# Kernel optimization log

Hardware: AMD Instinct MI355X
Metric: run time of the kernel (lower is better)

Reference implementation:

```python
import jax, jax.numpy as jnp
import numpy as np

BN_EPS = 1e-5
KNN_K = 9
HEAD = 4


def _bn(x, gamma, beta, axis=1):
    # eval-mode BatchNorm with running_mean=0, running_var=1
    shape = [1] * x.ndim
    shape[axis] = -1
    scale = (gamma / jnp.sqrt(1.0 + BN_EPS)).reshape(shape)
    return x * scale + beta.reshape(shape)


def _conv1d(x, W, b):
    # 1x1 Conv1d == channel matmul; x: [B,C,N], W: [O,C], b: [O]
    return jnp.einsum('oc,bcn->bon', W, x) + b[None, :, None]


def _knn_idx(x, k):
    # x: [B,C,N] -> idx [B,N,k] of k nearest (incl. self)
    xx = jnp.sum(x * x, axis=1)                      # [B,N]
    inner = jnp.einsum('bcn,bcm->bnm', x, x)         # [B,N,N]
    neg_d = 2.0 * inner - xx[:, :, None] - xx[:, None, :]
    return jax.lax.top_k(neg_d, k)[1]


def _graph_feature(x, k):
    # x: [B,C,N] -> [B,2C,N,k]  (cat of center feature and center - neighbor)
    B, C, N = x.shape
    idx = _knn_idx(x, k)                             # [B,N,k]
    xt = jnp.transpose(x, (0, 2, 1))                 # [B,N,C]
    nbr = jax.vmap(lambda xb, ib: xb[ib])(xt, idx)   # [B,N,k,C]
    ctr = jnp.broadcast_to(xt[:, :, None, :], (B, N, k, C))
    feat = jnp.concatenate([ctr, ctr - nbr], axis=3)  # [B,N,k,2C]
    return jnp.transpose(feat, (0, 3, 1, 2))


def _dgcnn_max(x, w1, b1, g1, be1, w2, b2, g2, be2, k):
    # x: [B,C,N] -> [B,C,N]; two 1x1 convs + BN + ReLU then max over k
    ef = _graph_feature(x, k)                        # [B,2C,N,k]
    h = jnp.einsum('oc,bcnk->bonk', w1, ef) + b1[None, :, None, None]
    h = jax.nn.relu(_bn(h, g1, be1, axis=1))
    h = jnp.einsum('oc,bcnk->bonk', w2, h) + b2[None, :, None, None]
    h = jax.nn.relu(_bn(h, g2, be2, axis=1))
    return jnp.max(h, axis=-1)                       # [B,C,N]


def _attention(m1, m2, wq, bq, wk, bk, wv, bv, wmh, bmh, wc1, bc1, cg, cbe, wc2, bc2):
    B, C, N = m1.shape
    hd = C // HEAD
    q = _conv1d(m1, wq, bq).reshape(B, HEAD, hd, N)
    kk = _conv1d(m2, wk, bk).reshape(B, HEAD, hd, -1)
    v = _conv1d(m2, wv, bv).reshape(B, HEAD, hd, -1)
    score = jax.nn.softmax(jnp.einsum('bhdn,bhdm->bhnm', q, kk) / (float(hd) ** 0.5), axis=-1)
    add = jnp.einsum('bhnm,bhdm->bhdn', score, v).reshape(B, C, N)
    add = _conv1d(add, wmh, bmh)
    cat = jnp.concatenate([m1, add], axis=1)         # [B,2C,N]
    h = jax.nn.relu(_bn(_conv1d(cat, wc1, bc1), cg, cbe, axis=1))
    return m1 + _conv1d(h, wc2, bc2)


def setup_inputs() -> dict:
    key = jax.random.key(0)
    B, C, N = 4, 128, 2000
    ks = jax.random.split(key, 24)

    def w(k, shape, s=0.05):
        return jax.random.normal(k, shape, dtype=jnp.float32) * s

    inp = {
        'x': jax.random.normal(ks[0], (B, C, N, 1), dtype=jnp.float32),
        'y': jax.random.normal(ks[1], (B, C, N), dtype=jnp.float32),
        # DGCNN_MAX_Block conv params (two 1x1 Conv2d + BN)
        'dg_w1': w(ks[2], (C, 2 * C)), 'dg_b1': w(ks[3], (C,)),
        'dg_g1': jnp.ones((C,), jnp.float32), 'dg_be1': jnp.zeros((C,), jnp.float32),
        'dg_w2': w(ks[4], (C, C)), 'dg_b2': w(ks[5], (C,)),
        'dg_g2': jnp.ones((C,), jnp.float32), 'dg_be2': jnp.zeros((C,), jnp.float32),
        # AttentionPropagation params
        'wq': w(ks[6], (C, C)), 'bq': w(ks[7], (C,)),
        'wk': w(ks[8], (C, C)), 'bk': w(ks[9], (C,)),
        'wv': w(ks[10], (C, C)), 'bv': w(ks[11], (C,)),
        'wmh': w(ks[12], (C, C)), 'bmh': w(ks[13], (C,)),
        'wc1': w(ks[14], (2 * C, 2 * C)), 'bc1': w(ks[15], (2 * C,)),
        'cg': jnp.ones((2 * C,), jnp.float32), 'cbe': jnp.zeros((2 * C,), jnp.float32),
        'wc2': w(ks[16], (C, 2 * C)), 'bc2': w(ks[17], (C,)),
    }
    return inp


def reference(x, y, dg_w1, dg_b1, dg_g1, dg_be1, dg_w2, dg_b2, dg_g2, dg_be2,
              wq, bq, wk, bk, wv, bv, wmh, bmh, wc1, bc1, cg, cbe, wc2, bc2):
    feats = x[:, :, :, 0]                            # [B,C,N]
    agg = _dgcnn_max(feats, dg_w1, dg_b1, dg_g1, dg_be1,
                     dg_w2, dg_b2, dg_g2, dg_be2, KNN_K)
    out = _attention(agg, y, wq, bq, wk, bk, wv, bv, wmh, bmh,
                     wc1, bc1, cg, cbe, wc2, bc2)
    return out[:, :, :, None]                        # [B,C,N,1]
```

## Files before the change

### kernel.cpp

```cpp
#include <hip/hip_runtime.h>

#define BATCH 4
#define CH    128
#define NPTS  2000
#define KNN   9
#define NHEAD 4
#define HD    32

typedef unsigned short u16;
typedef __attribute__((ext_vector_type(4))) float f32x4;
typedef __attribute__((ext_vector_type(8))) short bf16x8;

#define OFF_XT    0
#define OFF_YT    1024000
#define OFF_PT    2048000
#define OFF_QT    3072000
#define OFF_AGG   4096000
#define OFF_MH    5120000
#define OFF_MISC  6144000
#define OFF_W1SUM (OFF_MISC)
#define OFF_W1B   (OFF_MISC+16384)
#define OFF_W2T   (OFF_MISC+32768)
#define OFF_WC1T  (OFF_MISC+114688)
#define OFF_B1F   (OFF_MISC+212992)
#define OFF_B2F   (OFF_MISC+213120)
#define OFF_BC1F  (OFF_MISC+213248)
#define OFF_XX    (OFF_MISC+213504)
#define OFF_IDX   (OFF_MISC+221504)

__device__ __forceinline__ void bsplit(float v, u16& hi, u16& lo)
{
    unsigned u = __float_as_uint(v);
    unsigned h16 = (u + 0x7fffu + ((u >> 16) & 1u)) >> 16;
    float hf = __uint_as_float(h16 << 16);
    float lf = v - hf;
    unsigned ul = __float_as_uint(lf);
    hi = (u16)h16;
    lo = (u16)((ul + 0x7fffu + ((ul >> 16) & 1u)) >> 16);
}

__device__ __forceinline__ f32x4 mfma16(bf16x8 a, bf16x8 b, f32x4 c)
{
    return __builtin_amdgcn_mfma_f32_16x16x32_bf16(a, b, c, 0, 0, 0);
}

__global__ __launch_bounds__(256) void prep_kernel(
    const float* __restrict__ w1, const float* __restrict__ b1,
    const float* __restrict__ g1, const float* __restrict__ be1,
    const float* __restrict__ w2, const float* __restrict__ b2,
    const float* __restrict__ g2, const float* __restrict__ be2,
    const float* __restrict__ wc1, const float* __restrict__ bc1,
    const float* __restrict__ cg, const float* __restrict__ cbe,
    float* __restrict__ ws)
{
    int id = blockIdx.x * 256 + threadIdx.x;
    const float rs = rsqrtf(1.f + 1e-5f);
    if (id < 16384) {
        int o = id >> 7, c = id & 127;
        float s1 = g1[o] * rs;
        ws[OFF_W1SUM + id] = (w1[o*256 + c] + w1[o*256 + 128 + c]) * s1;
        ws[OFF_W1B   + id] = w1[o*256 + 128 + c] * s1;
        ws[OFF_W2T   + id] = w2[id] * (g2[o] * rs);
    }
    {
        int o = id >> 8;
        ws[OFF_WC1T + id] = wc1[id] * (cg[o] * rs);
    }
    if (id < 128) {
        float s1 = g1[id] * rs, s2 = g2[id] * rs;
        ws[OFF_B1F + id] = b1[id]*s1 + be1[id];
        ws[OFF_B2F + id] = b2[id]*s2 + be2[id];
    }
    if (id < 256) {
        ws[OFF_BC1F + id] = bc1[id]*(cg[id]*rs) + cbe[id];
    }
}

__global__ __launch_bounds__(128) void transpose_split_kernel(
    const float* __restrict__ src, float* __restrict__ dst, float* __restrict__ xx,
    u16* __restrict__ H, u16* __restrict__ L)
{
    int blk = blockIdx.x; int b = blk / NPTS, n = blk % NPTS;
    int c = threadIdx.x;
    float v = src[((size_t)b*CH + c)*NPTS + n];
    size_t di = ((size_t)b*NPTS + n)*CH + c;
    dst[di] = v;
    u16 hi, lo;
    bsplit(v, hi, lo);
    H[di] = hi; L[di] = lo;
    __shared__ float red[128];
    red[c] = v*v;
    __syncthreads();
    for (int s = 64; s > 0; s >>= 1) { if (c < s) red[c] += red[c+s]; __syncthreads(); }
    if (c == 0) xx[b*NPTS + n] = red[0];
}

__global__ __launch_bounds__(128) void transpose_kernel(
    const float* __restrict__ src, float* __restrict__ dst)
{
    int blk = blockIdx.x; int b = blk / NPTS, n = blk % NPTS;
    int c = threadIdx.x;
    dst[((size_t)b*NPTS + n)*CH + c] = src[((size_t)b*CH + c)*NPTS + n];
}

__global__ __launch_bounds__(512) void knn8_kernel(
    const u16* __restrict__ XH, const u16* __restrict__ XL,
    const float* __restrict__ xx, int* __restrict__ idxOut)
{
    __shared__ float woutv[8][16][9];
    __shared__ int   wouti[8][16][9];
    int b = blockIdx.y;
    int q0 = blockIdx.x * 16;
    int tid = threadIdx.x;
    int wave = tid >> 6, lane = tid & 63;
    int lg = lane >> 4, lr = lane & 15;
    const float* xxb = xx + (size_t)b*NPTS;

    size_t qb = ((size_t)b*NPTS + q0 + lr)*128 + lg*8;
    bf16x8 qh[4], ql[4];
#pragma unroll
    for (int ch = 0; ch < 4; ch++) {
        qh[ch] = *(const bf16x8*)&XH[qb + ch*32];
        ql[ch] = *(const bf16x8*)&XL[qb + ch*32];
    }

    float vals[4][9]; int ids[4][9];
    float vmin[4]; int amin[4];
#pragma unroll
    for (int j = 0; j < 4; j++) {
#pragma unroll
        for (int k = 0; k < 9; k++) { vals[j][k] = -3.4e38f; ids[j][k] = -1; }
        vmin[j] = -3.4e38f; amin[j] = 0;
    }

    for (int t = wave; t < 125; t += 8) {
        size_t kb = ((size_t)b*NPTS + t*16 + lr)*128 + lg*8;
        bf16x8 fh[4], fl[4];
#pragma unroll
        for (int ch = 0; ch < 4; ch++) {
            fh[ch] = *(const bf16x8*)&XH[kb + ch*32];
            fl[ch] = *(const bf16x8*)&XL[kb + ch*32];
        }
        float xv = xxb[t*16 + lr];
        f32x4 acc = {0.f,0.f,0.f,0.f};
#pragma unroll
        for (int ch = 0; ch < 4; ch++) {
            acc = mfma16(qh[ch], fh[ch], acc);
            acc = mfma16(qh[ch], fl[ch], acc);
            acc = mfma16(ql[ch], fh[ch], acc);
            acc = mfma16(ql[ch], fl[ch], acc);
        }
        int cand = t*16 + lr;
#pragma unroll
        for (int j = 0; j < 4; j++) {
            float s = 2.f*acc[j] - xv;
            if (s > vmin[j]) {
#pragma unroll
                for (int k = 0; k < 9; k++) {
                    bool sel = (k == amin[j]);
                    vals[j][k] = sel ? s    : vals[j][k];
                    ids[j][k]  = sel ? cand : ids[j][k];
                }
                vmin[j] = vals[j][0]; amin[j] = 0;
#pragma unroll
                for (int k = 1; k < 9; k++) {
                    bool lt = vals[j][k] < vmin[j];
                    vmin[j] = lt ? vals[j][k] : vmin[j];
                    amin[j] = lt ? k : amin[j];
                }
            }
        }
    }

#pragma unroll
    for (int j = 0; j < 4; j++) {
        unsigned used = 0;
        for (int r = 0; r < 9; r++) {
            float bv = -3.4e38f; int bm = -1;
#pragma unroll
            for (int k = 0; k < 9; k++) {
                bool ok = !(used & (1u << k)) && (vals[j][k] > bv);
                bv = ok ? vals[j][k] : bv;
                bm = ok ? ids[j][k]  : bm;
            }
            float v = bv; int mi = bm;
#pragma unroll
            for (int off = 1; off < 16; off <<= 1) {
                float ov = __shfl_xor(v, off);
                int  omi = __shfl_xor(mi, off);
                if (ov > v || (ov == v && omi >= 0 && omi < mi)) { v = ov; mi = omi; }
            }
#pragma unroll
            for (int k = 0; k < 9; k++) {
                if (ids[j][k] == mi) used |= (1u << k);
            }
            if (lr == 0) { woutv[wave][lg*4+j][r] = v; wouti[wave][lg*4+j][r] = mi; }
        }
    }
    __syncthreads();

    if (tid < 16) {
        float v0 = woutv[0][tid][0], v1 = woutv[1][tid][0], v2 = woutv[2][tid][0], v3 = woutv[3][tid][0];
        float v4 = woutv[4][tid][0], v5 = woutv[5][tid][0], v6 = woutv[6][tid][0], v7 = woutv[7][tid][0];
        int   i0 = wouti[0][tid][0], i1 = wouti[1][tid][0], i2 = wouti[2][tid][0], i3 = wouti[3][tid][0];
        int   i4 = wouti[4][tid][0], i5 = wouti[5][tid][0], i6 = wouti[6][tid][0], i7 = wouti[7][tid][0];
        int   p0 = 1, p1 = 1, p2 = 1, p3 = 1, p4 = 1, p5 = 1, p6 = 1, p7 = 1;
        int* op = idxOut + ((size_t)b*NPTS + q0 + tid)*KNN;
        for (int r = 0; r < 9; r++) {
            int w = 0; float bv = v0; int bi = i0;
            if (v1 > bv || (v1 == bv && i1 < bi)) { w = 1; bv = v1; bi = i1; }
            if (v2 > bv || (v2 == bv && i2 < bi)) { w = 2; bv = v2; bi = i2; }
            if (v3 > bv || (v3 == bv && i3 < bi)) { w = 3; bv = v3; bi = i3; }
            if (v4 > bv || (v4 == bv && i4 < bi)) { w = 4; bv = v4; bi = i4; }
            if (v5 > bv || (v5 == bv && i5 < bi)) { w = 5; bv = v5; bi = i5; }
            if (v6 > bv || (v6 == bv && i6 < bi)) { w = 6; bv = v6; bi = i6; }
            if (v7 > bv || (v7 == bv && i7 < bi)) { w = 7; bv = v7; bi = i7; }
            op[r] = bi;
            if (w == 0)      { v0 = (p0 < 9) ? woutv[0][tid][p0] : -3.4e38f; i0 = (p0 < 9) ? wouti[0][tid][p0] : 0x7fffffff; p0++; }
            else if (w == 1) { v1 = (p1 < 9) ? woutv[1][tid][p1] : -3.4e38f; i1 = (p1 < 9) ? wouti[1][tid][p1] : 0x7fffffff; p1++; }
            else if (w == 2) { v2 = (p2 < 9) ? woutv[2][tid][p2] : -3.4e38f; i2 = (p2 < 9) ? wouti[2][tid][p2] : 0x7fffffff; p2++; }
            else if (w == 3) { v3 = (p3 < 9) ? woutv[3][tid][p3] : -3.4e38f; i3 = (p3 < 9) ? wouti[3][tid][p3] : 0x7fffffff; p3++; }
            else if (w == 4) { v4 = (p4 < 9) ? woutv[4][tid][p4] : -3.4e38f; i4 = (p4 < 9) ? wouti[4][tid][p4] : 0x7fffffff; p4++; }
            else if (w == 5) { v5 = (p5 < 9) ? woutv[5][tid][p5] : -3.4e38f; i5 = (p5 < 9) ? wouti[5][tid][p5] : 0x7fffffff; p5++; }
            else if (w == 6) { v6 = (p6 < 9) ? woutv[6][tid][p6] : -3.4e38f; i6 = (p6 < 9) ? wouti[6][tid][p6] : 0x7fffffff; p6++; }
            else             { v7 = (p7 < 9) ? woutv[7][tid][p7] : -3.4e38f; i7 = (p7 < 9) ? wouti[7][tid][p7] : 0x7fffffff; p7++; }
        }
    }
}

__global__ __launch_bounds__(128) void gemm_dual_kernel(
    const float* __restrict__ In, const float* __restrict__ Wa, const float* __restrict__ Wb,
    const float* __restrict__ ba, const float* __restrict__ bb,
    float* __restrict__ OutA, float* __restrict__ OutB)
{
    __shared__ float in_lds[8][128];
    int row0 = blockIdx.x * 8, tid = threadIdx.x;
    const float* src = In + (size_t)row0 * 128;
    for (int i = tid; i < 1024; i += 128) ((float*)in_lds)[i] = src[i];
    __syncthreads();
    float accA[8], accB[8];
    float bA = ba ? ba[tid] : 0.f, bB = bb ? bb[tid] : 0.f;
#pragma unroll
    for (int j = 0; j < 8; j++) { accA[j] = bA; accB[j] = bB; }
    const float4* wra = (const float4*)(Wa + (size_t)tid * 128);
    const float4* wrb = (const float4*)(Wb + (size_t)tid * 128);
#pragma unroll 4
    for (int c4 = 0; c4 < 32; c4++) {
        float4 wa = wra[c4], wb = wrb[c4];
#pragma unroll
        for (int j = 0; j < 8; j++) {
            float4 xi = ((const float4*)&in_lds[j][0])[c4];
            accA[j] += xi.x*wa.x + xi.y*wa.y + xi.z*wa.z + xi.w*wa.w;
            accB[j] += xi.x*wb.x + xi.y*wb.y + xi.z*wb.z + xi.w*wb.w;
        }
    }
#pragma unroll
    for (int j = 0; j < 8; j++) {
        OutA[(size_t)(row0 + j)*128 + tid] = accA[j];
        OutB[(size_t)(row0 + j)*128 + tid] = accB[j];
    }
}

__global__ __launch_bounds__(128) void gemm_kv_kernel(
    const float* __restrict__ In, const float* __restrict__ Wa, const float* __restrict__ Wb,
    const float* __restrict__ ba, const float* __restrict__ bb,
    u16* __restrict__ KHo, u16* __restrict__ KLo,
    u16* __restrict__ VTHo, u16* __restrict__ VTLo)
{
    __shared__ float in_lds[8][128];
    int row0 = blockIdx.x * 8, tid = threadIdx.x;
    const float* src = In + (size_t)row0 * 128;
    for (int i = tid; i < 1024; i += 128) ((float*)in_lds)[i] = src[i];
    __syncthreads();
    float accA[8], accB[8];
    float bA = ba[tid], bB = bb[tid];
#pragma unroll
    for (int j = 0; j < 8; j++) { accA[j] = bA; accB[j] = bB; }
    const float4* wra = (const float4*)(Wa + (size_t)tid * 128);
    const float4* wrb = (const float4*)(Wb + (size_t)tid * 128);
#pragma unroll 4
    for (int c4 = 0; c4 < 32; c4++) {
        float4 wa = wra[c4], wb = wrb[c4];
#pragma unroll
        for (int j = 0; j < 8; j++) {
            float4 xi = ((const float4*)&in_lds[j][0])[c4];
            accA[j] += xi.x*wa.x + xi.y*wa.y + xi.z*wa.z + xi.w*wa.w;
            accB[j] += xi.x*wb.x + xi.y*wb.y + xi.z*wb.z + xi.w*wb.w;
        }
    }
    int b = row0 / NPTS, n0 = row0 % NPTS;
#pragma unroll
    for (int j = 0; j < 8; j++) {
        u16 hh, ll;
        bsplit(accA[j], hh, ll);
        size_t ko = (size_t)(row0 + j)*128 + tid;
        KHo[ko] = hh; KLo[ko] = ll;
        bsplit(accB[j], hh, ll);
        size_t vo = ((size_t)b*128 + tid)*NPTS + n0 + j;
        VTHo[vo] = hh; VTLo[vo] = ll;
    }
}

__global__ __launch_bounds__(128) void gemm_q_kernel(
    const float* __restrict__ In, const float* __restrict__ Wt, const float* __restrict__ bias,
    u16* __restrict__ H, u16* __restrict__ L)
{
    __shared__ float in_lds[8][128];
    int row0 = blockIdx.x * 8, tid = threadIdx.x;
    const float* src = In + (size_t)row0 * 128;
    for (int i = tid; i < 1024; i += 128) ((float*)in_lds)[i] = src[i];
    __syncthreads();
    float acc[8];
    float b = bias[tid];
#pragma unroll
    for (int j = 0; j < 8; j++) acc[j] = b;
    const float4* wrow = (const float4*)(Wt + (size_t)tid * 128);
#pragma unroll 4
    for (int c4 = 0; c4 < 32; c4++) {
        float4 w = wrow[c4];
#pragma unroll
        for (int j = 0; j < 8; j++) {
            float4 xi = ((const float4*)&in_lds[j][0])[c4];
            acc[j] += xi.x*w.x + xi.y*w.y + xi.z*w.z + xi.w*w.w;
        }
    }
#pragma unroll
    for (int j = 0; j < 8; j++) {
        u16 hh, ll;
        bsplit(acc[j], hh, ll);
        size_t o = (size_t)(row0 + j)*128 + tid;
        H[o] = hh; L[o] = ll;
    }
}

template<int CIN, int COUT, bool RELU, bool TRANSOUT, bool HASRES, bool CONCAT>
__global__ __launch_bounds__(COUT) void gemmT_kernel(
    const float* __restrict__ In, const float* __restrict__ In2,
    const float* __restrict__ Wt, const float* __restrict__ bias,
    const float* __restrict__ Res, float* __restrict__ Out)
{
    __shared__ float in_lds[8][CIN];
    int row0 = blockIdx.x * 8, tid = threadIdx.x;
    if (!CONCAT) {
        const float* src = In + (size_t)row0 * CIN;
        for (int i = tid; i < 8*CIN; i += COUT) ((float*)in_lds)[i] = src[i];
    } else {
        for (int i = tid; i < 8*128; i += COUT) {
            int j = i >> 7, c = i & 127;
            in_lds[j][c]       = In [(size_t)(row0 + j)*128 + c];
            in_lds[j][128 + c] = In2[(size_t)(row0 + j)*128 + c];
        }
    }
    __syncthreads();
    float acc[8];
    float b = bias ? bias[tid] : 0.f;
#pragma unroll
    for (int j = 0; j < 8; j++) acc[j] = b;
    const float4* wrow = (const float4*)(Wt + (size_t)tid * CIN);
#pragma unroll 4
    for (int c4 = 0; c4 < CIN/4; c4++) {
        float4 w = wrow[c4];
#pragma unroll
        for (int j = 0; j < 8; j++) {
            float4 xi = ((const float4*)&in_lds[j][0])[c4];
            acc[j] += xi.x*w.x + xi.y*w.y + xi.z*w.z + xi.w*w.w;
        }
    }
#pragma unroll
    for (int j = 0; j < 8; j++) {
        float v = acc[j];
        if (RELU) v = fmaxf(v, 0.f);
        size_t row = row0 + j;
        if (HASRES) v += Res[row*COUT + tid];
        if (!TRANSOUT) {
            Out[row*COUT + tid] = v;
        } else {
            int b_ = (int)(row / NPTS), n_ = (int)(row % NPTS);
            Out[((size_t)b_*COUT + tid)*NPTS + n_] = v;
        }
    }
}

__global__ __launch_bounds__(128) void edgeconv_kernel(
    const float* __restrict__ Pt, const float* __restrict__ Qt,
    const int* __restrict__ idx, const float* __restrict__ W2t,
    const float* __restrict__ b2f, float* __restrict__ Agg)
{
    int blk = blockIdx.x; int b = blk / NPTS, n = blk % NPTS;
    int o = threadIdx.x;
    __shared__ float r[9][128];
    __shared__ int mk[9];
    if (o < 9) mk[o] = idx[((size_t)b*NPTS + n)*KNN + o];
    __syncthreads();
    float p = Pt[((size_t)b*NPTS + n)*128 + o];
#pragma unroll
    for (int k = 0; k < 9; k++) {
        float q = Qt[((size_t)b*NPTS + mk[k])*128 + o];
        r[k][o] = fmaxf(p - q, 0.f);
    }
    __syncthreads();
    float acc[9];
#pragma unroll
    for (int k = 0; k < 9; k++) acc[k] = 0.f;
    const float4* w2row = (const float4*)(W2t + (size_t)o * 128);
#pragma unroll 2
    for (int c4 = 0; c4 < 32; c4++) {
        float4 w = w2row[c4];
#pragma unroll
        for (int k = 0; k < 9; k++) {
            float4 rv = ((const float4*)&r[k][0])[c4];
            acc[k] += rv.x*w.x + rv.y*w.y + rv.z*w.z + rv.w*w.w;
        }
    }
    float bb = b2f[o];
    float vmax = -3.4e38f;
#pragma unroll
    for (int k = 0; k < 9; k++) vmax = fmaxf(vmax, fmaxf(acc[k] + bb, 0.f));
    Agg[((size_t)b*NPTS + n)*128 + o] = vmax;
}

#define PSTR 72
__global__ __launch_bounds__(256) void attn_mfma_kernel(
    const u16* __restrict__ QH, const u16* __restrict__ QL,
    const u16* __restrict__ KH, const u16* __restrict__ KL,
    const u16* __restrict__ VTH, const u16* __restrict__ VTL,
    float* __restrict__ Add)
{
    __shared__ alignas(16) u16 Ph[4][16][PSTR];
    __shared__ alignas(16) u16 Pl[4][16][PSTR];
    int b = blockIdx.z, h = blockIdx.y;
    int wave = threadIdx.x >> 6, lane = threadIdx.x & 63;
    int lg = lane >> 4, lr = lane & 15;
    int q0 = blockIdx.x * 64 + wave * 16;
    if (q0 >= NPTS) return;

    size_t qb = ((size_t)b*NPTS + q0 + lr)*128 + h*32 + lg*8;
    const bf16x8 qh = *(const bf16x8*)&QH[qb];
    const bf16x8 ql = *(const bf16x8*)&QL[qb];

    f32x4 o0 = {0.f,0.f,0.f,0.f}, o1 = {0.f,0.f,0.f,0.f};
    float mrun[4], lsum[4];
#pragma unroll
    for (int r = 0; r < 4; r++) { mrun[r] = -3.0e38f; lsum[r] = 0.f; }
    const float sc = 0.17677669529663687f;
    int shsrc = ((lr >> 2) << 4) | (lr & 3);

    for (int ks = 0; ks < NPTS; ks += 64) {
        f32x4 st[4];
        bool vk[4];
#pragma unroll
        for (int s = 0; s < 4; s++) {
            int key = ks + s*16 + lr;
            vk[s] = key < NPTS;
            int kc = key > NPTS-1 ? NPTS-1 : key;
            size_t kb = ((size_t)b*NPTS + kc)*128 + h*32 + lg*8;
            bf16x8 kh_ = *(const bf16x8*)&KH[kb];
            bf16x8 kl_ = *(const bf16x8*)&KL[kb];
            f32x4 ss = {0.f,0.f,0.f,0.f};
            ss = mfma16(qh, kh_, ss);
            ss = mfma16(qh, kl_, ss);
            ss = mfma16(ql, kh_, ss);
            st[s] = ss;
        }
        float mx[4];
#pragma unroll
        for (int r = 0; r < 4; r++) {
            float m_ = -3.0e38f;
#pragma unroll
            for (int s = 0; s < 4; s++) {
                float a = vk[s] ? st[s][r]*sc : -3.0e38f;
                st[s][r] = a;
                m_ = fmaxf(m_, a);
            }
            mx[r] = m_;
        }
#pragma unroll
        for (int off = 1; off < 16; off <<= 1) {
#pragma unroll
            for (int r = 0; r < 4; r++) mx[r] = fmaxf(mx[r], __shfl_xor(mx[r], off));
        }
        float sca[4], rsu[4];
        float e[4][4];
#pragma unroll
        for (int r = 0; r < 4; r++) {
            float mn = fmaxf(mrun[r], mx[r]);
            sca[r] = __expf(mrun[r] - mn);
            mrun[r] = mn;
            float su = 0.f;
#pragma unroll
            for (int s = 0; s < 4; s++) {
                float ev = __expf(st[s][r] - mn);
                e[s][r] = ev;
                su += ev;
            }
            rsu[r] = su;
        }
#pragma unroll
        for (int off = 1; off < 16; off <<= 1) {
#pragma unroll
            for (int r = 0; r < 4; r++) rsu[r] += __shfl_xor(rsu[r], off);
        }
#pragma unroll
        for (int r = 0; r < 4; r++) lsum[r] = lsum[r]*sca[r] + rsu[r];
#pragma unroll
        for (int r = 0; r < 4; r++) {
            int qr = lg*4 + r;
#pragma unroll
            for (int s = 0; s < 4; s++) {
                u16 hh, ll;
                bsplit(e[s][r], hh, ll);
                Ph[wave][qr][s*16 + lr] = hh;
                Pl[wave][qr][s*16 + lr] = ll;
            }
        }
        float scsel = (lr & 2) ? ((lr & 1) ? sca[3] : sca[2])
                               : ((lr & 1) ? sca[1] : sca[0]);
        float osc = __shfl(scsel, shsrc);
#pragma unroll
        for (int r = 0; r < 4; r++) { o0[r] *= osc; o1[r] *= osc; }
#pragma unroll
        for (int c = 0; c < 2; c++) {
            int cb = ks + c*32 + lg*8; if (cb > NPTS-8) cb = NPTS-8;
            bf16x8 pbh = *(const bf16x8*)&Ph[wave][lr][c*32 + lg*8];
            bf16x8 pbl = *(const bf16x8*)&Pl[wave][lr][c*32 + lg*8];
            size_t vb = ((size_t)b*128 + h*32 + lr)*NPTS + cb;
            bf16x8 v0h = *(const bf16x8*)&VTH[vb];
            bf16x8 v0l = *(const bf16x8*)&VTL[vb];
            bf16x8 v1h = *(const bf16x8*)&VTH[vb + 16*NPTS];
            bf16x8 v1l = *(const bf16x8*)&VTL[vb + 16*NPTS];
            o0 = mfma16(v0h, pbh, o0);
            o0 = mfma16(v0l, pbh, o0);
            o0 = mfma16(v0h, pbl, o0);
            o1 = mfma16(v1h, pbh, o1);
            o1 = mfma16(v1l, pbh, o1);
            o1 = mfma16(v1h, pbl, o1);
        }
    }
    float lsel = (lr & 2) ? ((lr & 1) ? lsum[3] : lsum[2])
                          : ((lr & 1) ? lsum[1] : lsum[0]);
    float rinv = 1.f / __shfl(lsel, shsrc);
    int q = q0 + lr;
    size_t ob = ((size_t)b*NPTS + q)*128 + h*32;
#pragma unroll
    for (int r = 0; r < 4; r++) {
        Add[ob + lg*4 + r]      = o0[r]*rinv;
        Add[ob + 16 + lg*4 + r] = o1[r]*rinv;
    }
}

extern "C" void kernel_launch(void* const* d_in, const int* in_sizes, int n_in,
                              void* d_out, int out_size, void* d_ws, size_t ws_size,
                              hipStream_t stream)
{
    const float* x    = (const float*)d_in[0];
    const float* y    = (const float*)d_in[1];
    const float* w1   = (const float*)d_in[2];
    const float* b1   = (const float*)d_in[3];
    const float* g1   = (const float*)d_in[4];
    const float* be1  = (const float*)d_in[5];
    const float* w2   = (const float*)d_in[6];
    const float* b2   = (const float*)d_in[7];
    const float* g2   = (const float*)d_in[8];
    const float* be2  = (const float*)d_in[9];
    const float* wq   = (const float*)d_in[10];
    const float* bq   = (const float*)d_in[11];
    const float* wk   = (const float*)d_in[12];
    const float* bk   = (const float*)d_in[13];
    const float* wv   = (const float*)d_in[14];
    const float* bv   = (const float*)d_in[15];
    const float* wmh  = (const float*)d_in[16];
    const float* bmh  = (const float*)d_in[17];
    const float* wc1  = (const float*)d_in[18];
    const float* bc1  = (const float*)d_in[19];
    const float* cg   = (const float*)d_in[20];
    const float* cbe  = (const float*)d_in[21];
    const float* wc2  = (const float*)d_in[22];
    const float* bc2  = (const float*)d_in[23];
    float* ws = (float*)d_ws;
    float* out = (float*)d_out;

    float* XT  = ws + OFF_XT;
    float* YT  = ws + OFF_YT;
    float* PT  = ws + OFF_PT;
    float* QT  = ws + OFF_QT;
    float* AGG = ws + OFF_AGG;
    float* MH  = ws + OFF_MH;
    float* XX  = ws + OFF_XX;
    int*   IDX = (int*)(ws + OFF_IDX);
    float* ADD = YT;
    float* TT  = PT;
    const int SPE = BATCH*NPTS*CH;
    u16* XHs = (u16*)MH;  u16* XLs = XHs + SPE;
    u16* QHs = (u16*)MH;  u16* QLs = QHs + SPE;
    u16* KHs = (u16*)QT;  u16* KLs = KHs + SPE;
    u16* VTH = (u16*)PT;  u16* VTL = VTH + SPE;

    prep_kernel<<<256, 256, 0, stream>>>(w1, b1, g1, be1, w2, b2, g2, be2,
                                         wc1, bc1, cg, cbe, ws);
    transpose_split_kernel<<<BATCH*NPTS, 128, 0, stream>>>(x, XT, XX, XHs, XLs);
    transpose_kernel<<<BATCH*NPTS, 128, 0, stream>>>(y, YT);
    knn8_kernel<<<dim3(NPTS/16, BATCH), 512, 0, stream>>>(XHs, XLs, XX, IDX);
    gemm_dual_kernel<<<BATCH*NPTS/8, 128, 0, stream>>>(XT, ws + OFF_W1SUM, ws + OFF_W1B,
                                                       ws + OFF_B1F, nullptr, PT, QT);
    edgeconv_kernel<<<BATCH*NPTS, 128, 0, stream>>>(PT, QT, IDX, ws + OFF_W2T,
                                                    ws + OFF_B2F, AGG);
    gemm_q_kernel<<<BATCH*NPTS/8, 128, 0, stream>>>(AGG, wq, bq, QHs, QLs);
    gemm_kv_kernel<<<BATCH*NPTS/8, 128, 0, stream>>>(YT, wk, wv, bk, bv,
                                                     KHs, KLs, VTH, VTL);
    attn_mfma_kernel<<<dim3(32, NHEAD, BATCH), 256, 0, stream>>>(
        QHs, QLs, KHs, KLs, VTH, VTL, ADD);
    gemmT_kernel<128,128,false,false,false,false><<<BATCH*NPTS/8, 128, 0, stream>>>(
        ADD, nullptr, wmh, bmh, nullptr, MH);
    gemmT_kernel<256,256,true,false,false,true><<<BATCH*NPTS/8, 256, 0, stream>>>(
        AGG, MH, ws + OFF_WC1T, ws + OFF_BC1F, nullptr, TT);
    gemmT_kernel<256,128,false,true,true,false><<<BATCH*NPTS/8, 128, 0, stream>>>(
        TT, nullptr, wc2, bc2, AGG, out);
}
```

Baseline: 569.0 us.

## Split attention keys in two halves with merge kernel; halve GEMM row tiles

The attention kernel now splits the 2000 keys into two halves processed by separate blocks, writing unnormalized partial outputs plus running max/sum, and a new merge kernel combines them flash-decoding style. The attention inner loop is narrowed from 64 to 32 keys per step. All the row-tiled fp32 GEMM kernels process 4 rows per block instead of 8, doubling block counts. The intent is more parallelism and occupancy for the attention grid (128→256 blocks per batch-head set). The cost is an extra kernel, extra global traffic for partials, and less weight reuse per block in the GEMMs.

```diff
diff --git a/kernel.cpp b/kernel.cpp
--- a/kernel.cpp
+++ b/kernel.cpp
@@ -6,6 +6,7 @@
 #define KNN   9
 #define NHEAD 4
 #define HD    32
+#define NHALF 1000
 
 typedef unsigned short u16;
 typedef __attribute__((ext_vector_type(4))) float f32x4;
@@ -21,6 +22,7 @@
 #define OFF_W1SUM (OFF_MISC)
 #define OFF_W1B   (OFF_MISC+16384)
 #define OFF_W2T   (OFF_MISC+32768)
+#define OFF_ML0   (OFF_MISC+49152)
 #define OFF_WC1T  (OFF_MISC+114688)
 #define OFF_B1F   (OFF_MISC+212992)
 #define OFF_B2F   (OFF_MISC+213120)
@@ -56,7 +58,8 @@
     int id = blockIdx.x * 256 + threadIdx.x;
     const float rs = rsqrtf(1.f + 1e-5f);
     if (id < 16384) {
-        int o = id >> 7, c = id & 127;
+        int o = id >> 7;
+        int c = id & 127;
         float s1 = g1[o] * rs;
         ws[OFF_W1SUM + id] = (w1[o*256 + c] + w1[o*256 + 128 + c]) * s1;
         ws[OFF_W1B   + id] = w1[o*256 + 128 + c] * s1;
@@ -233,29 +236,29 @@
     const float* __restrict__ ba, const float* __restrict__ bb,
     float* __restrict__ OutA, float* __restrict__ OutB)
 {
-    __shared__ float in_lds[8][128];
-    int row0 = blockIdx.x * 8, tid = threadIdx.x;
+    __shared__ float in_lds[4][128];
+    int row0 = blockIdx.x * 4, tid = threadIdx.x;
     const float* src = In + (size_t)row0 * 128;
-    for (int i = tid; i < 1024; i += 128) ((float*)in_lds)[i] = src[i];
-    __syncthreads();
-    float accA[8], accB[8];
+    for (int i = tid; i < 512; i += 128) ((float*)in_lds)[i] = src[i];
+    __syncthreads();
+    float accA[4], accB[4];
     float bA = ba ? ba[tid] : 0.f, bB = bb ? bb[tid] : 0.f;
 #pragma unroll
-    for (int j = 0; j < 8; j++) { accA[j] = bA; accB[j] = bB; }
+    for (int j = 0; j < 4; j++) { accA[j] = bA; accB[j] = bB; }
     const float4* wra = (const float4*)(Wa + (size_t)tid * 128);
     const float4* wrb = (const float4*)(Wb + (size_t)tid * 128);
 #pragma unroll 4
     for (int c4 = 0; c4 < 32; c4++) {
         float4 wa = wra[c4], wb = wrb[c4];
 #pragma unroll
-        for (int j = 0; j < 8; j++) {
+        for (int j = 0; j < 4; j++) {
             float4 xi = ((const float4*)&in_lds[j][0])[c4];
             accA[j] += xi.x*wa.x + xi.y*wa.y + xi.z*wa.z + xi.w*wa.w;
             accB[j] += xi.x*wb.x + xi.y*wb.y + xi.z*wb.z + xi.w*wb.w;
         }
     }
 #pragma unroll
-    for (int j = 0; j < 8; j++) {
+    for (int j = 0; j < 4; j++) {
         OutA[(size_t)(row0 + j)*128 + tid] = accA[j];
         OutB[(size_t)(row0 + j)*128 + tid] = accB[j];
     }
@@ -267,22 +270,22 @@
     u16* __restrict__ KHo, u16* __restrict__ KLo,
     u16* __restrict__ VTHo, u16* __restrict__ VTLo)
 {
-    __shared__ float in_lds[8][128];
-    int row0 = blockIdx.x * 8, tid = threadIdx.x;
+    __shared__ float in_lds[4][128];
+    int row0 = blockIdx.x * 4, tid = threadIdx.x;
     const float* src = In + (size_t)row0 * 128;
-    for (int i = tid; i < 1024; i += 128) ((float*)in_lds)[i] = src[i];
-    __syncthreads();
-    float accA[8], accB[8];
+    for (int i = tid; i < 512; i += 128) ((float*)in_lds)[i] = src[i];
+    __syncthreads();
+    float accA[4], accB[4];
     float bA = ba[tid], bB = bb[tid];
 #pragma unroll
-    for (int j = 0; j < 8; j++) { accA[j] = bA; accB[j] = bB; }
+    for (int j = 0; j < 4; j++) { accA[j] = bA; accB[j] = bB; }
     const float4* wra = (const float4*)(Wa + (size_t)tid * 128);
     const float4* wrb = (const float4*)(Wb + (size_t)tid * 128);
 #pragma unroll 4
     for (int c4 = 0; c4 < 32; c4++) {
         float4 wa = wra[c4], wb = wrb[c4];
 #pragma unroll
-        for (int j = 0; j < 8; j++) {
+        for (int j = 0; j < 4; j++) {
             float4 xi = ((const float4*)&in_lds[j][0])[c4];
             accA[j] += xi.x*wa.x + xi.y*wa.y + xi.z*wa.z + xi.w*wa.w;
             accB[j] += xi.x*wb.x + xi.y*wb.y + xi.z*wb.z + xi.w*wb.w;
@@ -290,7 +293,7 @@
     }
     int b = row0 / NPTS, n0 = row0 % NPTS;
 #pragma unroll
-    for (int j = 0; j < 8; j++) {
+    for (int j = 0; j < 4; j++) {
         u16 hh, ll;
         bsplit(accA[j], hh, ll);
         size_t ko = (size_t)(row0 + j)*128 + tid;
@@ -305,27 +308,27 @@
     const float* __restrict__ In, const float* __restrict__ Wt, const float* __restrict__ bias,
     u16* __restrict__ H, u16* __restrict__ L)
 {
-    __shared__ float in_lds[8][128];
-    int row0 = blockIdx.x * 8, tid = threadIdx.x;
+    __shared__ float in_lds[4][128];
+    int row0 = blockIdx.x * 4, tid = threadIdx.x;
     const float* src = In + (size_t)row0 * 128;
-    for (int i = tid; i < 1024; i += 128) ((float*)in_lds)[i] = src[i];
-    __syncthreads();
-    float acc[8];
+    for (int i = tid; i < 512; i += 128) ((float*)in_lds)[i] = src[i];
+    __syncthreads();
+    float acc[4];
     float b = bias[tid];
 #pragma unroll
-    for (int j = 0; j < 8; j++) acc[j] = b;
+    for (int j = 0; j < 4; j++) acc[j] = b;
     const float4* wrow = (const float4*)(Wt + (size_t)tid * 128);
 #pragma unroll 4
     for (int c4 = 0; c4 < 32; c4++) {
         float4 w = wrow[c4];
 #pragma unroll
-        for (int j = 0; j < 8; j++) {
+        for (int j = 0; j < 4; j++) {
             float4 xi = ((const float4*)&in_lds[j][0])[c4];
             acc[j] += xi.x*w.x + xi.y*w.y + xi.z*w.z + xi.w*w.w;
         }
     }
 #pragma unroll
-    for (int j = 0; j < 8; j++) {
+    for (int j = 0; j < 4; j++) {
         u16 hh, ll;
         bsplit(acc[j], hh, ll);
         size_t o = (size_t)(row0 + j)*128 + tid;
@@ -339,35 +342,35 @@
     const float* __restrict__ Wt, const float* __restrict__ bias,
     const float* __restrict__ Res, float* __restrict__ Out)
 {
-    __shared__ float in_lds[8][CIN];
-    int row0 = blockIdx.x * 8, tid = threadIdx.x;
+    __shared__ float in_lds[4][CIN];
+    int row0 = blockIdx.x * 4, tid = threadIdx.x;
     if (!CONCAT) {
         const float* src = In + (size_t)row0 * CIN;
-        for (int i = tid; i < 8*CIN; i += COUT) ((float*)in_lds)[i] = src[i];
+        for (int i = tid; i < 4*CIN; i += COUT) ((float*)in_lds)[i] = src[i];
     } else {
-        for (int i = tid; i < 8*128; i += COUT) {
+        for (int i = tid; i < 4*128; i += COUT) {
             int j = i >> 7, c = i & 127;
             in_lds[j][c]       = In [(size_t)(row0 + j)*128 + c];
             in_lds[j][128 + c] = In2[(size_t)(row0 + j)*128 + c];
         }
     }
     __syncthreads();
-    float acc[8];
+    float acc[4];
     float b = bias ? bias[tid] : 0.f;
 #pragma unroll
-    for (int j = 0; j < 8; j++) acc[j] = b;
+    for (int j = 0; j < 4; j++) acc[j] = b;
     const float4* wrow = (const float4*)(Wt + (size_t)tid * CIN);
 #pragma unroll 4
     for (int c4 = 0; c4 < CIN/4; c4++) {
         float4 w = wrow[c4];
 #pragma unroll
-        for (int j = 0; j < 8; j++) {
+        for (int j = 0; j < 4; j++) {
             float4 xi = ((const float4*)&in_lds[j][0])[c4];
             acc[j] += xi.x*w.x + xi.y*w.y + xi.z*w.z + xi.w*w.w;
         }
     }
 #pragma unroll
-    for (int j = 0; j < 8; j++) {
+    for (int j = 0; j < 4; j++) {
         float v = acc[j];
         if (RELU) v = fmaxf(v, 0.f);
         size_t row = row0 + j;
@@ -424,15 +427,20 @@
     const u16* __restrict__ QH, const u16* __restrict__ QL,
     const u16* __restrict__ KH, const u16* __restrict__ KL,
     const u16* __restrict__ VTH, const u16* __restrict__ VTL,
-    float* __restrict__ Add)
+    float* __restrict__ O0, float* __restrict__ O1,
+    float* __restrict__ ML0, float* __restrict__ ML1)
 {
     __shared__ alignas(16) u16 Ph[4][16][PSTR];
     __shared__ alignas(16) u16 Pl[4][16][PSTR];
     int b = blockIdx.z, h = blockIdx.y;
+    int split = blockIdx.x & 1, qt = blockIdx.x >> 1;
     int wave = threadIdx.x >> 6, lane = threadIdx.x & 63;
     int lg = lane >> 4, lr = lane & 15;
-    int q0 = blockIdx.x * 64 + wave * 16;
+    int q0 = qt * 64 + wave * 16;
     if (q0 >= NPTS) return;
+    int kstart = split * NHALF, kend = kstart + NHALF;
+    float* Op = split ? O1 : O0;
+    float* ml = split ? ML1 : ML0;
 
     size_t qb = ((size_t)b*NPTS + q0 + lr)*128 + h*32 + lg*8;
     const bf16x8 qh = *(const bf16x8*)&QH[qb];
@@ -445,55 +453,44 @@
     const float sc = 0.17677669529663687f;
     int shsrc = ((lr >> 2) << 4) | (lr & 3);
 
-    for (int ks = 0; ks < NPTS; ks += 64) {
-        f32x4 st[4];
-        bool vk[4];
-#pragma unroll
-        for (int s = 0; s < 4; s++) {
-            int key = ks + s*16 + lr;
-            vk[s] = key < NPTS;
-            int kc = key > NPTS-1 ? NPTS-1 : key;
-            size_t kb = ((size_t)b*NPTS + kc)*128 + h*32 + lg*8;
-            bf16x8 kh_ = *(const bf16x8*)&KH[kb];
-            bf16x8 kl_ = *(const bf16x8*)&KL[kb];
-            f32x4 ss = {0.f,0.f,0.f,0.f};
-            ss = mfma16(qh, kh_, ss);
-            ss = mfma16(qh, kl_, ss);
-            ss = mfma16(ql, kh_, ss);
-            st[s] = ss;
-        }
+    for (int ks = kstart; ks < kend; ks += 32) {
+        int k0i = ks + lr;      bool vk0 = k0i < kend; if (k0i > kend-1) k0i = kend-1;
+        int k1i = ks + 16 + lr; bool vk1 = k1i < kend; if (k1i > kend-1) k1i = kend-1;
+        size_t kb0 = ((size_t)b*NPTS + k0i)*128 + h*32 + lg*8;
+        size_t kb1 = ((size_t)b*NPTS + k1i)*128 + h*32 + lg*8;
+        bf16x8 k0h = *(const bf16x8*)&KH[kb0];
+        bf16x8 k0l = *(const bf16x8*)&KL[kb0];
+        bf16x8 k1h = *(const bf16x8*)&KH[kb1];
+        bf16x8 k1l = *(const bf16x8*)&KL[kb1];
+        f32x4 s0 = {0.f,0.f,0.f,0.f}, s1 = {0.f,0.f,0.f,0.f};
+        s0 = mfma16(qh, k0h, s0);
+        s0 = mfma16(qh, k0l, s0);
+        s0 = mfma16(ql, k0h, s0);
+        s1 = mfma16(qh, k1h, s1);
+        s1 = mfma16(qh, k1l, s1);
+        s1 = mfma16(ql, k1h, s1);
         float mx[4];
 #pragma unroll
         for (int r = 0; r < 4; r++) {
-            float m_ = -3.0e38f;
-#pragma unroll
-            for (int s = 0; s < 4; s++) {
-                float a = vk[s] ? st[s][r]*sc : -3.0e38f;
-                st[s][r] = a;
-                m_ = fmaxf(m_, a);
-            }
-            mx[r] = m_;
+            float a  = vk0 ? s0[r]*sc : -3.0e38f;
+            float a2 = vk1 ? s1[r]*sc : -3.0e38f;
+            s0[r] = a; s1[r] = a2;
+            mx[r] = fmaxf(a, a2);
         }
 #pragma unroll
         for (int off = 1; off < 16; off <<= 1) {
 #pragma unroll
             for (int r = 0; r < 4; r++) mx[r] = fmaxf(mx[r], __shfl_xor(mx[r], off));
         }
-        float sca[4], rsu[4];
-        float e[4][4];
+        float e0[4], e1[4], rsu[4], sca[4];
 #pragma unroll
         for (int r = 0; r < 4; r++) {
             float mn = fmaxf(mrun[r], mx[r]);
             sca[r] = __expf(mrun[r] - mn);
             mrun[r] = mn;
-            float su = 0.f;
-#pragma unroll
-            for (int s = 0; s < 4; s++) {
-                float ev = __expf(st[s][r] - mn);
-                e[s][r] = ev;
-                su += ev;
-            }
-            rsu[r] = su;
+            e0[r] = __expf(s0[r] - mn);
+            e1[r] = __expf(s1[r] - mn);
+            rsu[r] = e0[r] + e1[r];
         }
 #pragma unroll
         for (int off = 1; off < 16; off <<= 1) {
@@ -504,48 +501,68 @@
         for (int r = 0; r < 4; r++) lsum[r] = lsum[r]*sca[r] + rsu[r];
 #pragma unroll
         for (int r = 0; r < 4; r++) {
+            u16 h0, w0, h1, w1;
+            bsplit(e0[r], h0, w0);
+            bsplit(e1[r], h1, w1);
             int qr = lg*4 + r;
-#pragma unroll
-            for (int s = 0; s < 4; s++) {
-                u16 hh, ll;
-                bsplit(e[s][r], hh, ll);
-                Ph[wave][qr][s*16 + lr] = hh;
-                Pl[wave][qr][s*16 + lr] = ll;
-            }
+            Ph[wave][qr][lr]      = h0;
+            Pl[wave][qr][lr]      = w0;
+            Ph[wave][qr][16 + lr] = h1;
+            Pl[wave][qr][16 + lr] = w1;
         }
         float scsel = (lr & 2) ? ((lr & 1) ? sca[3] : sca[2])
                                : ((lr & 1) ? sca[1] : sca[0]);
         float osc = __shfl(scsel, shsrc);
 #pragma unroll
         for (int r = 0; r < 4; r++) { o0[r] *= osc; o1[r] *= osc; }
-#pragma unroll
-        for (int c = 0; c < 2; c++) {
-            int cb = ks + c*32 + lg*8; if (cb > NPTS-8) cb = NPTS-8;
-            bf16x8 pbh = *(const bf16x8*)&Ph[wave][lr][c*32 + lg*8];
-            bf16x8 pbl = *(const bf16x8*)&Pl[wave][lr][c*32 + lg*8];
-            size_t vb = ((size_t)b*128 + h*32 + lr)*NPTS + cb;
-            bf16x8 v0h = *(const bf16x8*)&VTH[vb];
-            bf16x8 v0l = *(const bf16x8*)&VTL[vb];
-            bf16x8 v1h = *(const bf16x8*)&VTH[vb + 16*NPTS];
-            bf16x8 v1l = *(const bf16x8*)&VTL[vb + 16*NPTS];
-            o0 = mfma16(v0h, pbh, o0);
-            o0 = mfma16(v0l, pbh, o0);
-            o0 = mfma16(v0h, pbl, o0);
-            o1 = mfma16(v1h, pbh, o1);
-            o1 = mfma16(v1l, pbh, o1);
-            o1 = mfma16(v1h, pbl, o1);
-        }
-    }
-    float lsel = (lr & 2) ? ((lr & 1) ? lsum[3] : lsum[2])
-                          : ((lr & 1) ? lsum[1] : lsum[0]);
-    float rinv = 1.f / __shfl(lsel, shsrc);
+        int cb = ks + lg*8; if (cb > kend-8) cb = kend-8;
+        bf16x8 pbh = *(const bf16x8*)&Ph[wave][lr][lg*8];
+        bf16x8 pbl = *(const bf16x8*)&Pl[wave][lr][lg*8];
+        size_t vb = ((size_t)b*128 + h*32 + lr)*NPTS + cb;
+        bf16x8 v0h = *(const bf16x8*)&VTH[vb];
+        bf16x8 v0l = *(const bf16x8*)&VTL[vb];
+        bf16x8 v1h = *(const bf16x8*)&VTH[vb + 16*NPTS];
+        bf16x8 v1l = *(const bf16x8*)&VTL[vb + 16*NPTS];
+        o0 = mfma16(v0h, pbh, o0);
+        o0 = mfma16(v0l, pbh, o0);
+        o0 = mfma16(v0h, pbl, o0);
+        o1 = mfma16(v1h, pbh, o1);
+        o1 = mfma16(v1l, pbh, o1);
+        o1 = mfma16(v1h, pbl, o1);
+    }
+    if (lr == 0) {
+#pragma unroll
+        for (int r = 0; r < 4; r++) {
+            size_t mo = (((size_t)b*NHEAD + h)*NPTS + q0 + lg*4 + r)*2;
+            ml[mo]   = mrun[r];
+            ml[mo+1] = lsum[r];
+        }
+    }
     int q = q0 + lr;
     size_t ob = ((size_t)b*NPTS + q)*128 + h*32;
 #pragma unroll
     for (int r = 0; r < 4; r++) {
-        Add[ob + lg*4 + r]      = o0[r]*rinv;
-        Add[ob + 16 + lg*4 + r] = o1[r]*rinv;
-    }
+        Op[ob + lg*4 + r]      = o0[r];
+        Op[ob + 16 + lg*4 + r] = o1[r];
+    }
+}
+
+__global__ __launch_bounds__(256) void attn_merge_kernel(
+    const float* __restrict__ O0, const float* __restrict__ ML0,
+    const float* __restrict__ ML1, float* __restrict__ O1 )
+{
+    int id = blockIdx.x * 256 + threadIdx.x;
+    int c = id & 127;
+    int q = (id >> 7) % NPTS;
+    int b = id / (NPTS * 128);
+    int h = c >> 5;
+    size_t mo = (((size_t)b*NHEAD + h)*NPTS + q)*2;
+    float m0 = ML0[mo], l0 = ML0[mo+1];
+    float m1 = ML1[mo], l1 = ML1[mo+1];
+    float M = fmaxf(m0, m1);
+    float w0 = __expf(m0 - M), w1 = __expf(m1 - M);
+    float inv = 1.f / (l0*w0 + l1*w1);
+    O1[id] = (O0[id]*w0 + O1[id]*w1) * inv;
 }
 
 extern "C" void kernel_launch(void* const* d_in, const int* in_sizes, int n_in,
@@ -587,7 +604,11 @@
     float* MH  = ws + OFF_MH;
     float* XX  = ws + OFF_XX;
     int*   IDX = (int*)(ws + OFF_IDX);
+    float* O0s = XT;
+    float* O1s = YT;
     float* ADD = YT;
+    float* ML0 = ws + OFF_ML0;
+    float* ML1 = ws + OFF_XX;
     float* TT  = PT;
     const int SPE = BATCH*NPTS*CH;
     u16* XHs = (u16*)MH;  u16* XLs = XHs + SPE;
@@ -600,19 +621,20 @@
     transpose_split_kernel<<<BATCH*NPTS, 128, 0, stream>>>(x, XT, XX, XHs, XLs);
     transpose_kernel<<<BATCH*NPTS, 128, 0, stream>>>(y, YT);
     knn8_kernel<<<dim3(NPTS/16, BATCH), 512, 0, stream>>>(XHs, XLs, XX, IDX);
-    gemm_dual_kernel<<<BATCH*NPTS/8, 128, 0, stream>>>(XT, ws + OFF_W1SUM, ws + OFF_W1B,
+    gemm_dual_kernel<<<BATCH*NPTS/4, 128, 0, stream>>>(XT, ws + OFF_W1SUM, ws + OFF_W1B,
                                                        ws + OFF_B1F, nullptr, PT, QT);
     edgeconv_kernel<<<BATCH*NPTS, 128, 0, stream>>>(PT, QT, IDX, ws + OFF_W2T,
                                                     ws + OFF_B2F, AGG);
-    gemm_q_kernel<<<BATCH*NPTS/8, 128, 0, stream>>>(AGG, wq, bq, QHs, QLs);
-    gemm_kv_kernel<<<BATCH*NPTS/8, 128, 0, stream>>>(YT, wk, wv, bk, bv,
+    gemm_q_kernel<<<BATCH*NPTS/4, 128, 0, stream>>>(AGG, wq, bq, QHs, QLs);
+    gemm_kv_kernel<<<BATCH*NPTS/4, 128, 0, stream>>>(YT, wk, wv, bk, bv,
                                                      KHs, KLs, VTH, VTL);
-    attn_mfma_kernel<<<dim3(32, NHEAD, BATCH), 256, 0, stream>>>(
-        QHs, QLs, KHs, KLs, VTH, VTL, ADD);
-    gemmT_kernel<128,128,false,false,false,false><<<BATCH*NPTS/8, 128, 0, stream>>>(
+    attn_mfma_kernel<<<dim3(64, NHEAD, BATCH), 256, 0, stream>>>(
+        QHs, QLs, KHs, KLs, VTH, VTL, O0s, O1s, ML0, ML1);
+    attn_merge_kernel<<<BATCH*NPTS*CH/256, 256, 0, stream>>>(O0s, ML0, ML1, O1s);
+    gemmT_kernel<128,128,false,false,false,false><<<BATCH*NPTS/4, 128, 0, stream>>>(
         ADD, nullptr, wmh, bmh, nullptr, MH);
-    gemmT_kernel<256,256,true,false,false,true><<<BATCH*NPTS/8, 256, 0, stream>>>(
+    gemmT_kernel<256,256,true,false,false,true><<<BATCH*NPTS/4, 256, 0, stream>>>(
         AGG, MH, ws + OFF_WC1T, ws + OFF_BC1F, nullptr, TT);
-    gemmT_kernel<256,128,false,true,true,false><<<BATCH*NPTS/8, 128, 0, stream>>>(
+    gemmT_kernel<256,128,false,true,true,false><<<BATCH*NPTS/4, 128, 0, stream>>>(
         TT, nullptr, wc2, bc2, AGG, out);
 }
```

Result: slower. 605.8 us (+6.5%).
